# Kernel optimization log

Hardware: AMD Instinct MI355X
Metric: run time of the kernel (lower is better)

## Reference

```python
import jax, jax.numpy as jnp
import numpy as np

IM_SIZE = (256, 256)
GRID_SIZE = (512, 512)
J = 6                    # numpoints per dim
L = 1024                 # table oversampling
ALPHA = 2.34 * J         # Kaiser-Bessel alpha (order 0)
CENTER = J * L // 2      # center index of the KB table
B, C, M = 2, 16, 409600  # batch, coils, k-space points


def _kb_ft(f, J_, alpha):
    """Fourier transform of the order-0 Kaiser-Bessel kernel (Fessler)."""
    z = np.sqrt((np.pi * J_ * f) ** 2 - alpha ** 2 + 0j)
    z = np.where(np.abs(z) < 1e-12, 1e-12, z)
    return np.real(J_ * np.sinh(z) / (z * np.i0(alpha)))


def _build_table(J_, L_, K, N, alpha):
    """Oversampled KB kernel table with the linear phase that centers the
    apodization at (N-1)/2 (torchkbnufft stores complex tables for this reason)."""
    u = (np.arange(J_ * L_ + 1) - J_ * L_ / 2.0) / L_  # grid-unit offsets in [-J/2, J/2]
    fr = np.sqrt(np.maximum(0.0, 1.0 - (2.0 * u / J_) ** 2))
    kb = np.where(np.abs(u) <= J_ / 2.0, np.i0(alpha * fr) / np.i0(alpha), 0.0)
    tab = kb * np.exp(-1j * (2.0 * np.pi / K) * u * (N - 1) / 2.0)
    return np.stack([tab.real, tab.imag]).astype(np.float32)


def setup_inputs():
    key = jax.random.key(0)
    k1, k2 = jax.random.split(key)
    x = jax.random.normal(k1, (B, C, 2) + IM_SIZE, dtype=jnp.float32)
    om = jax.random.uniform(k2, (B, 2, M), dtype=jnp.float32, minval=-jnp.pi, maxval=jnp.pi)
    scs = []
    for d in range(2):
        n = np.arange(IM_SIZE[d]) - (IM_SIZE[d] - 1) / 2.0
        scs.append(1.0 / _kb_ft(n / GRID_SIZE[d], J, ALPHA))
    sc = np.outer(scs[0], scs[1])
    scaling_coef = jnp.asarray(np.stack([sc, np.zeros_like(sc)]).astype(np.float32))
    table_0 = jnp.asarray(_build_table(J, L, GRID_SIZE[0], IM_SIZE[0], ALPHA))
    table_1 = jnp.asarray(_build_table(J, L, GRID_SIZE[1], IM_SIZE[1], ALPHA))
    n_shift = jnp.asarray(np.array([IM_SIZE[0] // 2, IM_SIZE[1] // 2], dtype=np.float32))
    return {"x": x, "om": om, "scaling_coef": scaling_coef,
            "table_0": table_0, "table_1": table_1, "n_shift": n_shift}


def reference(x, om, scaling_coef, table_0, table_1, n_shift):
    K0, K1 = GRID_SIZE
    # apodize by scaling coefficients, zero-pad to the oversampled grid, FFT
    xc = (x[:, :, 0] + 1j * x[:, :, 1]) * (scaling_coef[0] + 1j * scaling_coef[1])
    xc = jnp.pad(xc, ((0, 0), (0, 0), (0, K0 - IM_SIZE[0]), (0, K1 - IM_SIZE[1])))
    Gf = jnp.fft.fftn(xc, axes=(-2, -1)).reshape(xc.shape[0], xc.shape[1], K0 * K1)
    t0 = table_0[0] + 1j * table_0[1]
    t1 = table_1[0] + 1j * table_1[1]
    # fractional grid coordinates of the off-grid points
    tm0 = om[:, 0] * (K0 / (2.0 * jnp.pi))  # (B, M)
    tm1 = om[:, 1] * (K1 / (2.0 * jnp.pi))
    koff0 = jnp.floor(tm0 - J / 2.0).astype(jnp.int32) + 1
    koff1 = jnp.floor(tm1 - J / 2.0).astype(jnp.int32) + 1
    # per-dim table-lookup coefficients and wrapped grid indices
    c0, i0, c1, i1 = [], [], [], []
    for j in range(J):
        g0 = koff0 + j
        g1 = koff1 + j
        c0.append(t0[jnp.round((tm0 - g0) * L).astype(jnp.int32) + CENTER])
        c1.append(t1[jnp.round((tm1 - g1) * L).astype(jnp.int32) + CENTER])
        i0.append(jnp.mod(g0, K0))
        i1.append(jnp.mod(g1, K1))
    # separable J x J neighbor accumulation (matches Jlist loop in torchkbnufft)
    kdat = jnp.zeros((Gf.shape[0], Gf.shape[1], tm0.shape[-1]), dtype=Gf.dtype)
    for a in range(J):
        for b in range(J):
            idx = (i0[a] * K1 + i1[b])[:, None, :]          # (B, 1, M)
            vals = jnp.take_along_axis(Gf, idx, axis=2)     # (B, C, M) gather
            kdat = kdat + (c0[a] * c1[b])[:, None, :] * vals
    # fftshift phase
    phase = jnp.exp(1j * (om[:, 0] * n_shift[0] + om[:, 1] * n_shift[1]))
    kdat = kdat * phase[:, None, :]
    return jnp.stack([kdat.real, kdat.imag], axis=2)  # (B, C, 2, M)
```

## Files before the change

kernel.cpp:

```cpp
#include <hip/hip_runtime.h>
#include <math.h>

#define BB 2
#define CC 16
#define MM 409600
#define NI 256
#define JJ 6
#define TABLE_LEN 6145
#define CENTER 3072
#define TILE 16
#define TDIM 32
#define NTILES 1024
#define HALO 22
#define HSZ (HALO * HALO)
#define NBINS 2048
#define CAP 640
#define BINC_STRIDE 16
#define SC_PPB 4096
#define SC_THREADS 1024
#define SC_PPT 4
#define GRP 4
#define NGRP 4
#define SB_THREADS 256
#define SB_PPT 3

__global__ void fft512_row_fused(const float* __restrict__ x, const float* __restrict__ sc,
                                 float2* __restrict__ gf, int b) {
  __shared__ float2 bufA[512];
  __shared__ float2 bufB[512];
  int line = blockIdx.x;
  int c = line >> 8;
  int gi = line & 255;
  int t = threadIdx.x;
  float2* g = gf + (((size_t)c << 9) | gi) * 512;
  const float* xb = x + (size_t)(b * CC + c) * 2 * NI * NI + gi * NI;
  float xr = xb[t];
  float xi = xb[NI * NI + t];
  const float* scb = sc + gi * NI;
  float sr = scb[t];
  float si = scb[NI * NI + t];
  bufA[t] = make_float2(xr * sr - xi * si, xr * si + xi * sr);
  bufA[t + 256] = make_float2(0.f, 0.f);
  __syncthreads();
  float2* X = bufA;
  float2* Y = bufB;
  const float C0 = -6.283185307179586f / 512.0f;
  #pragma unroll
  for (int k = 0; k < 9; ++k) {
    int s = 1 << k;
    float2 a = X[t];
    float2 bb = X[t + 256];
    int ps = t & ~(s - 1);
    float ang = C0 * (float)ps;
    float wr, wi;
    __sincosf(ang, &wi, &wr);
    int wbase = ((t >> k) << (k + 1)) | (t & (s - 1));
    float2 dif = make_float2(a.x - bb.x, a.y - bb.y);
    Y[wbase] = make_float2(a.x + bb.x, a.y + bb.y);
    Y[wbase + s] = make_float2(dif.x * wr - dif.y * wi, dif.x * wi + dif.y * wr);
    __syncthreads();
    float2* tmp = X; X = Y; Y = tmp;
  }
  g[t] = X[t];
  g[t + 256] = X[t + 256];
}

__global__ void fft512_col(float2* __restrict__ data) {
  __shared__ float2 bufA[512 * 8];
  __shared__ float2 bufB[512 * 8];
  int blk = blockIdx.x;
  int img = blk >> 6;
  int cg = blk & 63;
  float2* g = data + ((size_t)img << 18) + cg * 8;
  int t = threadIdx.x;
  int col = t & 7;
  int r0 = t >> 3;
  #pragma unroll
  for (int k = 0; k < 2; ++k) {
    int row = r0 + 128 * k;
    bufA[row * 8 + col] = g[(size_t)row * 512 + col];
  }
  #pragma unroll
  for (int k = 2; k < 4; ++k) {
    int row = r0 + 128 * k;
    bufA[row * 8 + col] = make_float2(0.f, 0.f);
  }
  __syncthreads();
  float2* X = bufA;
  float2* Y = bufB;
  const float C0 = -6.283185307179586f / 512.0f;
  #pragma unroll
  for (int k = 0; k < 9; ++k) {
    int s = 1 << k;
    #pragma unroll
    for (int h = 0; h < 2; ++h) {
      int j = r0 + 128 * h;
      float2 a = X[j * 8 + col];
      float2 b = X[(j + 256) * 8 + col];
      int ps = j & ~(s - 1);
      float ang = C0 * (float)ps;
      float wr, wi;
      __sincosf(ang, &wi, &wr);
      int wbase = ((j >> k) << (k + 1)) | (j & (s - 1));
      float2 dif = make_float2(a.x - b.x, a.y - b.y);
      Y[wbase * 8 + col] = make_float2(a.x + b.x, a.y + b.y);
      Y[(wbase + s) * 8 + col] = make_float2(dif.x * wr - dif.y * wi, dif.x * wi + dif.y * wr);
    }
    __syncthreads();
    float2* tmp = X; X = Y; Y = tmp;
  }
  #pragma unroll
  for (int k = 0; k < 4; ++k) {
    int row = r0 + 128 * k;
    g[(size_t)row * 512 + col] = X[row * 8 + col];
  }
}

__global__ void prep(const float* __restrict__ t0, const float* __restrict__ t1,
                     float2* __restrict__ tab0, float2* __restrict__ tab1,
                     int* __restrict__ binc) {
  int i = blockIdx.x * blockDim.x + threadIdx.x;
  if (i < TABLE_LEN) {
    tab0[i] = make_float2(t0[i], t0[TABLE_LEN + i]);
    tab1[i] = make_float2(t1[i], t1[TABLE_LEN + i]);
  }
  if (i < NBINS * BINC_STRIDE) binc[i] = 0;
}

__global__ void scatter_points(const float* __restrict__ om,
                               int* __restrict__ binc,
                               float2* __restrict__ bpts, int* __restrict__ invcap) {
  __shared__ int lhist[NBINS];
  __shared__ int lbase[NBINS];
  __shared__ int lpos[NBINS];
  int t = threadIdx.x;
  int bid = blockIdx.x;
  for (int i = t; i < NBINS; i += SC_THREADS) { lhist[i] = 0; lpos[i] = 0; }
  __syncthreads();
  const float scale = 81.48733086305042f;
  float ptm0[SC_PPT], ptm1[SC_PPT];
  int pbin[SC_PPT];
  #pragma unroll
  for (int i = 0; i < SC_PPT; ++i) {
    int idx = bid * SC_PPB + i * SC_THREADS + t;
    int b = idx / MM;
    int m = idx - b * MM;
    float om0 = om[(size_t)b * 2 * MM + m];
    float om1 = om[(size_t)b * 2 * MM + MM + m];
    float tm0 = om0 * scale;
    float tm1 = om1 * scale;
    int s0 = ((int)floorf(tm0 - 3.0f) + 1) & 511;
    int s1 = ((int)floorf(tm1 - 3.0f) + 1) & 511;
    int bin = b * NTILES + (s0 >> 4) * TDIM + (s1 >> 4);
    ptm0[i] = tm0; ptm1[i] = tm1;
    pbin[i] = bin;
    atomicAdd(&lhist[bin], 1);
  }
  __syncthreads();
  for (int i = t; i < NBINS; i += SC_THREADS)
    lbase[i] = atomicAdd(&binc[i * BINC_STRIDE], lhist[i]);
  __syncthreads();
  #pragma unroll
  for (int i = 0; i < SC_PPT; ++i) {
    int idx = bid * SC_PPB + i * SC_THREADS + t;
    int bin = pbin[i];
    int pos = atomicAdd(&lpos[bin], 1);
    int slot = lbase[bin] + pos;
    if (slot < CAP) {
      bpts[bin * CAP + slot] = make_float2(ptm0[i], ptm1[i]);
    }
    int sl = slot < CAP ? slot : CAP - 1;
    invcap[idx] = (bin << 10) | sl;
  }
}

__global__ void prefix_bins(const int* __restrict__ binc, int* __restrict__ dbase) {
  __shared__ int buf[NBINS];
  int t = threadIdx.x;
  int c0 = binc[t * BINC_STRIDE];
  c0 = c0 < 0 ? 0 : (c0 > CAP ? CAP : c0);
  int c1 = binc[(NTILES + t) * BINC_STRIDE];
  c1 = c1 < 0 ? 0 : (c1 > CAP ? CAP : c1);
  buf[t] = c0;
  buf[NTILES + t] = c1;
  __syncthreads();
  for (int off = 1; off < NTILES; off <<= 1) {
    int v0 = (t >= off) ? buf[t - off] : 0;
    int v1 = (t >= off) ? buf[NTILES + t - off] : 0;
    __syncthreads();
    buf[t] += v0;
    buf[NTILES + t] += v1;
    __syncthreads();
  }
  dbase[t] = buf[t] - c0;
  dbase[NTILES + t] = buf[NTILES + t] - c1;
}

__global__ void sort_bins(float2* __restrict__ bpts, const int* __restrict__ binc,
                          unsigned short* __restrict__ perm) {
  __shared__ int hist[256];
  int bin = blockIdx.x;
  int t = threadIdx.x;
  int n = binc[bin * BINC_STRIDE];
  n = n < 0 ? 0 : (n > CAP ? CAP : n);
  hist[t] = 0;
  __syncthreads();
  float2 pts[SB_PPT];
  int keys[SB_PPT];
  #pragma unroll
  for (int i = 0; i < SB_PPT; ++i) {
    int p = t + i * SB_THREADS;
    keys[i] = -1;
    if (p < n) {
      float2 pt = bpts[bin * CAP + p];
      int d0 = (((int)floorf(pt.x - 3.0f)) + 1) & 15;
      int d1 = (((int)floorf(pt.y - 3.0f)) + 1) & 15;
      keys[i] = (d0 << 4) | d1;
      pts[i] = pt;
      atomicAdd(&hist[keys[i]], 1);
    }
  }
  __syncthreads();
  int c = hist[t];
  for (int off = 1; off < 256; off <<= 1) {
    int u = (t >= off) ? hist[t - off] : 0;
    __syncthreads();
    hist[t] += u;
    __syncthreads();
  }
  int excl = hist[t] - c;
  __syncthreads();
  hist[t] = excl;
  __syncthreads();
  #pragma unroll
  for (int i = 0; i < SB_PPT; ++i) {
    if (keys[i] >= 0) {
      int np = atomicAdd(&hist[keys[i]], 1);
      bpts[bin * CAP + np] = pts[i];
      perm[bin * CAP + (t + i * SB_THREADS)] = (unsigned short)np;
    }
  }
}

__global__ void __launch_bounds__(256, 4)
interp_binned(const float2* __restrict__ gf,
              const float2* __restrict__ bpts,
              const int* __restrict__ binc,
              const int* __restrict__ dbase,
              const float2* __restrict__ tab0,
              const float2* __restrict__ tab1,
              float2* __restrict__ tmp, int b) {
  __shared__ float2 lds[GRP * HSZ];
  int blk = blockIdx.x;
  int grp = blk & (NGRP - 1);
  int tile = blk >> 2;
  int cbase = grp * GRP;
  int tile0 = tile >> 5, tile1 = tile & 31;
  int base0 = tile0 * TILE, base1 = tile1 * TILE;
  int tid = threadIdx.x;
  for (int i = tid; i < GRP * HSZ; i += 256) {
    int cc = i / HSZ;
    int rem = i - cc * HSZ;
    int r = rem / HALO;
    int cl = rem - r * HALO;
    const float2* img = gf + ((size_t)(cbase + cc) << 18);
    lds[i] = img[(((base0 + r) & 511) << 9) | ((base1 + cl) & 511)];
  }
  __syncthreads();
  int bin = b * NTILES + tile;
  int count = binc[bin * BINC_STRIDE];
  count = count < 0 ? 0 : (count > CAP ? CAP : count);
  int pbase = bin * CAP;
  int dbin = dbase[bin];
  for (int p = tid; p < count; p += 256) {
    float2 pt = bpts[pbase + p];
    float tm0 = pt.x, tm1 = pt.y;
    int koff0 = (int)floorf(tm0 - 3.0f) + 1;
    int koff1 = (int)floorf(tm1 - 3.0f) + 1;
    int d0 = koff0 & 15;
    int d1 = koff1 & 15;
    float c0r[JJ], c0i[JJ], c1r[JJ], c1i[JJ];
    #pragma unroll
    for (int j = 0; j < JJ; ++j) {
      int idx0 = (int)rintf((tm0 - (float)(koff0 + j)) * 1024.0f) + CENTER;
      idx0 = idx0 < 0 ? 0 : (idx0 > TABLE_LEN - 1 ? TABLE_LEN - 1 : idx0);
      float2 v0 = tab0[idx0];
      c0r[j] = v0.x; c0i[j] = v0.y;
      int idx1 = (int)rintf((tm1 - (float)(koff1 + j)) * 1024.0f) + CENTER;
      idx1 = idx1 < 0 ? 0 : (idx1 > TABLE_LEN - 1 ? TABLE_LEN - 1 : idx1);
      float2 v1 = tab1[idx1];
      c1r[j] = v1.x; c1i[j] = v1.y;
    }
    float2 res[GRP];
    #pragma unroll
    for (int g = 0; g < GRP; ++g) {
      const float2* hal = lds + g * HSZ;
      float ar = 0.f, ai = 0.f;
      #pragma unroll
      for (int ja = 0; ja < JJ; ++ja) {
        const float2* row = hal + (d0 + ja) * HALO + d1;
        float rr = 0.f, ri = 0.f;
        #pragma unroll
        for (int jb = 0; jb < JJ; ++jb) {
          float2 v = row[jb];
          rr += c1r[jb] * v.x - c1i[jb] * v.y;
          ri += c1r[jb] * v.y + c1i[jb] * v.x;
        }
        ar += c0r[ja] * rr - c0i[ja] * ri;
        ai += c0r[ja] * ri + c0i[ja] * rr;
      }
      res[g] = make_float2(ar, ai);
    }
    float4* d4 = (float4*)(tmp + ((size_t)grp * MM + (dbin + p)) * GRP);
    d4[0] = make_float4(res[0].x, res[0].y, res[1].x, res[1].y);
    d4[1] = make_float4(res[2].x, res[2].y, res[3].x, res[3].y);
  }
}

__global__ void gather_out(const float2* __restrict__ tmp, const int* __restrict__ invcap,
                           const int* __restrict__ dbase, const unsigned short* __restrict__ perm,
                           const float* __restrict__ om,
                           const float* __restrict__ nshift, float* __restrict__ out, int b) {
  int m = blockIdx.x * blockDim.x + threadIdx.x;
  if (m >= MM) return;
  int v = invcap[b * MM + m];
  int bin = v >> 10;
  int pos = v & 1023;
  int slot = dbase[bin] + (int)perm[bin * CAP + pos];
  float om0 = om[(size_t)b * 2 * MM + m];
  float om1 = om[(size_t)b * 2 * MM + MM + m];
  float ph = om0 * nshift[0] + om1 * nshift[1];
  float sp, cp;
  __sincosf(ph, &sp, &cp);
  float* ob = out + (size_t)b * CC * 2 * MM + m;
  #pragma unroll
  for (int g = 0; g < NGRP; ++g) {
    const float4* src = (const float4*)(tmp + ((size_t)g * MM + slot) * GRP);
    float4 v0 = src[0];
    float4 v1 = src[1];
    int c = g * GRP;
    ob[(size_t)(2 * c + 0) * MM] = v0.x * cp - v0.y * sp;
    ob[(size_t)(2 * c + 1) * MM] = v0.x * sp + v0.y * cp;
    ob[(size_t)(2 * c + 2) * MM] = v0.z * cp - v0.w * sp;
    ob[(size_t)(2 * c + 3) * MM] = v0.z * sp + v0.w * cp;
    ob[(size_t)(2 * c + 4) * MM] = v1.x * cp - v1.y * sp;
    ob[(size_t)(2 * c + 5) * MM] = v1.x * sp + v1.y * cp;
    ob[(size_t)(2 * c + 6) * MM] = v1.z * cp - v1.w * sp;
    ob[(size_t)(2 * c + 7) * MM] = v1.z * sp + v1.w * cp;
  }
}

extern "C" void kernel_launch(void* const* d_in, const int* in_sizes, int n_in,
                              void* d_out, int out_size, void* d_ws, size_t ws_size,
                              hipStream_t stream) {
  const float* x = (const float*)d_in[0];
  const float* om = (const float*)d_in[1];
  const float* sc = (const float*)d_in[2];
  const float* t0 = (const float*)d_in[3];
  const float* t1 = (const float*)d_in[4];
  const float* nshift = (const float*)d_in[5];
  float* out = (float*)d_out;

  char* ws = (char*)d_ws;
  float2* gf = (float2*)ws;
  size_t off = (size_t)CC * 512 * 512 * sizeof(float2);
  float2* bpts = (float2*)(ws + off); off += (size_t)NBINS * CAP * sizeof(float2);
  float2* tmp = (float2*)(ws + off);  off += (size_t)MM * CC * sizeof(float2);
  int* invcap = (int*)(ws + off);     off += (size_t)BB * MM * sizeof(int);
  unsigned short* perm = (unsigned short*)(ws + off); off += (size_t)NBINS * CAP * sizeof(unsigned short);
  float2* tab0 = (float2*)(ws + off); off += (size_t)TABLE_LEN * sizeof(float2);
  float2* tab1 = (float2*)(ws + off); off += (size_t)TABLE_LEN * sizeof(float2);
  int* binc = (int*)(ws + off);       off += (size_t)NBINS * BINC_STRIDE * sizeof(int);
  int* dbase = (int*)(ws + off);      off += (size_t)NBINS * sizeof(int);

  prep<<<(NBINS * BINC_STRIDE + 255) / 256, 256, 0, stream>>>(t0, t1, tab0, tab1, binc);
  scatter_points<<<BB * MM / SC_PPB, SC_THREADS, 0, stream>>>(om, binc, bpts, invcap);
  prefix_bins<<<1, NTILES, 0, stream>>>(binc, dbase);
  sort_bins<<<NBINS, SB_THREADS, 0, stream>>>(bpts, binc, perm);
  for (int b = 0; b < BB; ++b) {
    fft512_row_fused<<<CC * 256, 256, 0, stream>>>(x, sc, gf, b);
    fft512_col<<<CC * 64, 1024, 0, stream>>>(gf);
    interp_binned<<<NTILES * NGRP, 256, 0, stream>>>(gf, bpts, binc, dbase, tab0, tab1, tmp, b);
    gather_out<<<MM / 256, 256, 0, stream>>>(tmp, invcap, dbase, perm, om, nshift, out, b);
  }
}
```

Baseline: 457.8 us.

## Batch both images into single kernel launches and interleave tmp by coil

When the workspace is large enough, the per-batch loop is replaced by single launches that cover both batch items, with the gf and tmp buffers doubled. This removes launch gaps and tail underutilisation across the four per-batch kernels. The tmp layout changes from group-major to point-major with all 16 coils contiguous, so gather_out reads one contiguous 128-byte chunk per point. The cost is twice the workspace footprint. It also assumes fft512_col indexes correctly across the doubled grid count, which is not visible here.

```diff
diff --git a/kernel.cpp b/kernel.cpp
--- a/kernel.cpp
+++ b/kernel.cpp
@@ -25,14 +25,17 @@
 #define SB_PPT 3
 
 __global__ void fft512_row_fused(const float* __restrict__ x, const float* __restrict__ sc,
-                                 float2* __restrict__ gf, int b) {
+                                 float2* __restrict__ gf, int b0) {
   __shared__ float2 bufA[512];
   __shared__ float2 bufB[512];
-  int line = blockIdx.x;
+  int blk = blockIdx.x;
+  int bloc = blk >> 12;
+  int line = blk & 4095;
   int c = line >> 8;
   int gi = line & 255;
+  int b = b0 + bloc;
   int t = threadIdx.x;
-  float2* g = gf + (((size_t)c << 9) | gi) * 512;
+  float2* g = gf + ((size_t)bloc * CC << 18) + (((size_t)c << 9) | gi) * 512;
   const float* xb = x + (size_t)(b * CC + c) * 2 * NI * NI + gi * NI;
   float xr = xb[t];
   float xi = xb[NI * NI + t];
@@ -249,21 +252,26 @@
               const int* __restrict__ dbase,
               const float2* __restrict__ tab0,
               const float2* __restrict__ tab1,
-              float2* __restrict__ tmp, int b) {
+              float2* __restrict__ tmp, int b0) {
   __shared__ float2 lds[GRP * HSZ];
   int blk = blockIdx.x;
-  int grp = blk & (NGRP - 1);
-  int tile = blk >> 2;
+  int bloc = blk >> 12;
+  int lb = blk & 4095;
+  int grp = lb & (NGRP - 1);
+  int tile = lb >> 2;
+  int b = b0 + bloc;
   int cbase = grp * GRP;
   int tile0 = tile >> 5, tile1 = tile & 31;
   int base0 = tile0 * TILE, base1 = tile1 * TILE;
   int tid = threadIdx.x;
+  const float2* gfb = gf + ((size_t)bloc * CC << 18);
+  float2* tmpb = tmp + (size_t)bloc * MM * CC;
   for (int i = tid; i < GRP * HSZ; i += 256) {
     int cc = i / HSZ;
     int rem = i - cc * HSZ;
     int r = rem / HALO;
     int cl = rem - r * HALO;
-    const float2* img = gf + ((size_t)(cbase + cc) << 18);
+    const float2* img = gfb + ((size_t)(cbase + cc) << 18);
     lds[i] = img[(((base0 + r) & 511) << 9) | ((base1 + cl) & 511)];
   }
   __syncthreads();
@@ -311,7 +319,7 @@
       }
       res[g] = make_float2(ar, ai);
     }
-    float4* d4 = (float4*)(tmp + ((size_t)grp * MM + (dbin + p)) * GRP);
+    float4* d4 = (float4*)(tmpb + (size_t)(dbin + p) * CC + cbase);
     d4[0] = make_float4(res[0].x, res[0].y, res[1].x, res[1].y);
     d4[1] = make_float4(res[2].x, res[2].y, res[3].x, res[3].y);
   }
@@ -320,9 +328,11 @@
 __global__ void gather_out(const float2* __restrict__ tmp, const int* __restrict__ invcap,
                            const int* __restrict__ dbase, const unsigned short* __restrict__ perm,
                            const float* __restrict__ om,
-                           const float* __restrict__ nshift, float* __restrict__ out, int b) {
-  int m = blockIdx.x * blockDim.x + threadIdx.x;
-  if (m >= MM) return;
+                           const float* __restrict__ nshift, float* __restrict__ out, int b0) {
+  int idx = blockIdx.x * blockDim.x + threadIdx.x;
+  int bloc = idx >= MM ? 1 : 0;
+  int m = idx - bloc * MM;
+  int b = b0 + bloc;
   int v = invcap[b * MM + m];
   int bin = v >> 10;
   int pos = v & 1023;
@@ -332,21 +342,21 @@
   float ph = om0 * nshift[0] + om1 * nshift[1];
   float sp, cp;
   __sincosf(ph, &sp, &cp);
+  const float2* tmpb = tmp + (size_t)bloc * MM * CC;
+  const float4* src = (const float4*)(tmpb + (size_t)slot * CC);
   float* ob = out + (size_t)b * CC * 2 * MM + m;
   #pragma unroll
-  for (int g = 0; g < NGRP; ++g) {
-    const float4* src = (const float4*)(tmp + ((size_t)g * MM + slot) * GRP);
-    float4 v0 = src[0];
-    float4 v1 = src[1];
-    int c = g * GRP;
-    ob[(size_t)(2 * c + 0) * MM] = v0.x * cp - v0.y * sp;
-    ob[(size_t)(2 * c + 1) * MM] = v0.x * sp + v0.y * cp;
-    ob[(size_t)(2 * c + 2) * MM] = v0.z * cp - v0.w * sp;
-    ob[(size_t)(2 * c + 3) * MM] = v0.z * sp + v0.w * cp;
-    ob[(size_t)(2 * c + 4) * MM] = v1.x * cp - v1.y * sp;
-    ob[(size_t)(2 * c + 5) * MM] = v1.x * sp + v1.y * cp;
-    ob[(size_t)(2 * c + 6) * MM] = v1.z * cp - v1.w * sp;
-    ob[(size_t)(2 * c + 7) * MM] = v1.z * sp + v1.w * cp;
+  for (int k = 0; k < 8; ++k) {
+    float4 v4 = src[k];
+    float r0 = v4.x * cp - v4.y * sp;
+    float i0 = v4.x * sp + v4.y * cp;
+    float r1 = v4.z * cp - v4.w * sp;
+    float i1 = v4.z * sp + v4.w * cp;
+    int c = 2 * k;
+    ob[(size_t)(2 * c) * MM] = r0;
+    ob[(size_t)(2 * c + 1) * MM] = i0;
+    ob[(size_t)(2 * c + 2) * MM] = r1;
+    ob[(size_t)(2 * c + 3) * MM] = i1;
   }
 }
 
@@ -361,11 +371,21 @@
   const float* nshift = (const float*)d_in[5];
   float* out = (float*)d_out;
 
+  const size_t gf_one = (size_t)CC * 512 * 512 * sizeof(float2);
+  const size_t tmp_one = (size_t)MM * CC * sizeof(float2);
+  const size_t fixed = (size_t)NBINS * CAP * sizeof(float2)
+                     + (size_t)BB * MM * sizeof(int)
+                     + (size_t)NBINS * CAP * sizeof(unsigned short)
+                     + 2 * (size_t)TABLE_LEN * sizeof(float2)
+                     + (size_t)NBINS * BINC_STRIDE * sizeof(int)
+                     + (size_t)NBINS * sizeof(int) + 4096;
+  int nb = (ws_size >= fixed + 2 * (gf_one + tmp_one)) ? 2 : 1;
+
   char* ws = (char*)d_ws;
   float2* gf = (float2*)ws;
-  size_t off = (size_t)CC * 512 * 512 * sizeof(float2);
+  size_t off = (size_t)nb * gf_one;
+  float2* tmp = (float2*)(ws + off);  off += (size_t)nb * tmp_one;
   float2* bpts = (float2*)(ws + off); off += (size_t)NBINS * CAP * sizeof(float2);
-  float2* tmp = (float2*)(ws + off);  off += (size_t)MM * CC * sizeof(float2);
   int* invcap = (int*)(ws + off);     off += (size_t)BB * MM * sizeof(int);
   unsigned short* perm = (unsigned short*)(ws + off); off += (size_t)NBINS * CAP * sizeof(unsigned short);
   float2* tab0 = (float2*)(ws + off); off += (size_t)TABLE_LEN * sizeof(float2);
@@ -377,10 +397,18 @@
   scatter_points<<<BB * MM / SC_PPB, SC_THREADS, 0, stream>>>(om, binc, bpts, invcap);
   prefix_bins<<<1, NTILES, 0, stream>>>(binc, dbase);
   sort_bins<<<NBINS, SB_THREADS, 0, stream>>>(bpts, binc, perm);
-  for (int b = 0; b < BB; ++b) {
-    fft512_row_fused<<<CC * 256, 256, 0, stream>>>(x, sc, gf, b);
-    fft512_col<<<CC * 64, 1024, 0, stream>>>(gf);
-    interp_binned<<<NTILES * NGRP, 256, 0, stream>>>(gf, bpts, binc, dbase, tab0, tab1, tmp, b);
-    gather_out<<<MM / 256, 256, 0, stream>>>(tmp, invcap, dbase, perm, om, nshift, out, b);
-  }
-}
+
+  if (nb == 2) {
+    fft512_row_fused<<<2 * CC * 256, 256, 0, stream>>>(x, sc, gf, 0);
+    fft512_col<<<2 * CC * 64, 1024, 0, stream>>>(gf);
+    interp_binned<<<2 * NTILES * NGRP, 256, 0, stream>>>(gf, bpts, binc, dbase, tab0, tab1, tmp, 0);
+    gather_out<<<2 * MM / 256, 256, 0, stream>>>(tmp, invcap, dbase, perm, om, nshift, out, 0);
+  } else {
+    for (int b = 0; b < BB; ++b) {
+      fft512_row_fused<<<CC * 256, 256, 0, stream>>>(x, sc, gf, b);
+      fft512_col<<<CC * 64, 1024, 0, stream>>>(gf);
+      interp_binned<<<NTILES * NGRP, 256, 0, stream>>>(gf, bpts, binc, dbase, tab0, tab1, tmp, b);
+      gather_out<<<MM / 256, 256, 0, stream>>>(tmp, invcap, dbase, perm, om, nshift, out, b);
+    }
+  }
+}
```

Result: faster. 405.5 us (-11.4%).
